# Kernel tuning notes

Hardware: AMD Instinct MI355X
Metric: run time of the kernel (lower is better)

## Reference

```python
import jax, jax.numpy as jnp
import numpy as np
import math

DIM = 1024
HEADS = 16
HEAD_DIM = DIM // HEADS
ROT = min(HEAD_DIM, 32)  # rotary_dim
B, S = 2, 1024


def setup_inputs() -> dict:
    key = jax.random.key(0)
    ks = jax.random.split(key, 32)
    lin = lambda k: jax.random.normal(k, (DIM, DIM), jnp.float32) * 0.02
    bias = lambda k: jax.random.normal(k, (DIM,), jnp.float32) * 0.01
    inp = {
        'real': jax.random.normal(ks[0], (B, S, DIM), jnp.float32),
        'imag': jax.random.normal(ks[1], (B, S, DIM), jnp.float32),
        'Wq_r': lin(ks[2]), 'bq_r': bias(ks[3]),
        'Wk_r': lin(ks[4]), 'bk_r': bias(ks[5]),
        'Wv_r': lin(ks[6]), 'bv_r': bias(ks[7]),
        'Wq_i': lin(ks[8]), 'bq_i': bias(ks[9]),
        'Wk_i': lin(ks[10]), 'bk_i': bias(ks[11]),
        'Wv_i': lin(ks[12]), 'bv_i': bias(ks[13]),
        'Wo_r': lin(ks[14]), 'bo_r': bias(ks[15]),
        'Wo_i': lin(ks[16]), 'bo_i': bias(ks[17]),
        'phase_shifts': jax.random.normal(ks[18], (HEADS, HEAD_DIM), jnp.float32) * 0.02,
        'ent': jnp.eye(HEADS, dtype=jnp.float32) + jax.random.normal(ks[19], (HEADS, HEADS), jnp.float32) * 0.01,
        'rot_freqs': (10000.0 ** (-jnp.arange(0, ROT, 2, dtype=jnp.float32) / ROT)),
        'strength': jnp.ones((1,), jnp.float32),
        'temp': jnp.ones((1,), jnp.float32),
    }
    return inp


def _fwd(real, imag, Wq_r, bq_r, Wk_r, bk_r, Wv_r, bv_r,
         Wq_i, bq_i, Wk_i, bk_i, Wv_i, bv_i,
         Wo_r, bo_r, Wo_i, bo_i,
         phase_shifts, ent, rot_freqs, strength, temp):
    b, s, _ = real.shape
    to_heads = lambda t: t.reshape(b, s, HEADS, HEAD_DIM).transpose(0, 2, 1, 3)  # bhsd
    lin = lambda x, W, bb: x @ W + bb

    q_r = to_heads(lin(real, Wq_r, bq_r))
    k_r = to_heads(lin(real, Wk_r, bk_r))
    v_r = to_heads(lin(real, Wv_r, bv_r))
    q_i = to_heads(lin(imag, Wq_i, bq_i))
    k_i = to_heads(lin(imag, Wk_i, bk_i))
    v_i = to_heads(lin(imag, Wv_i, bv_i))

    # rotary on first ROT dims (pairwise rotation)
    pos = jnp.arange(s, dtype=jnp.float32)
    emb = pos[:, None] * rot_freqs[None, :]           # [S, ROT/2]
    cos = jnp.cos(emb)[None, None]                    # [1,1,S,ROT/2]
    sin = jnp.sin(emb)[None, None]

    def rope(t):
        tr = t[..., :ROT].reshape(b, HEADS, s, ROT // 2, 2)
        r0 = tr[..., 0] * cos - tr[..., 1] * sin
        r1 = tr[..., 1] * cos + tr[..., 0] * sin
        rr = jnp.stack([r0, r1], axis=-1).reshape(b, HEADS, s, ROT)
        return jnp.concatenate([rr, t[..., ROT:]], axis=-1)

    q_r, k_r = rope(q_r), rope(k_r)
    q_i, k_i = rope(q_i), rope(k_i)

    # entanglement mixing across heads
    mix = lambda t: jnp.einsum('bhsd,hx->bxsd', t, ent)
    q_r, q_i, k_r, k_i = mix(q_r), mix(q_i), mix(k_r), mix(k_i)

    # per-head phase shift (complex rotation)
    pc = jnp.cos(phase_shifts)[None, :, None, :]      # [1,H,1,D]
    ps = jnp.sin(phase_shifts)[None, :, None, :]
    q_r, q_i = q_r * pc - q_i * ps, q_r * ps + q_i * pc
    k_r, k_i = k_r * pc - k_i * ps, k_r * ps + k_i * pc

    scale = 1.0 / math.sqrt(HEAD_DIM)
    attn_r = (jnp.einsum('bhqd,bhkd->bhqk', q_r, k_r) + jnp.einsum('bhqd,bhkd->bhqk', q_i, k_i)) * scale
    attn_i = (jnp.einsum('bhqd,bhkd->bhqk', q_i, k_r) - jnp.einsum('bhqd,bhkd->bhqk', q_r, k_i)) * scale
    attn_mag = jnp.sqrt(attn_r ** 2 + attn_i ** 2 + 1e-6)

    causal = jnp.triu(jnp.ones((s, s), dtype=bool), k=1)[None, None]
    attn_mag = jnp.where(causal, -jnp.inf, attn_mag)

    t = jnp.maximum(temp, 0.01)
    g = jax.nn.sigmoid(strength)
    attn = jax.nn.softmax(attn_mag * g / t, axis=-1)

    out_r = jnp.einsum('bhqk,bhkd->bhqd', attn, v_r).transpose(0, 2, 1, 3).reshape(b, s, DIM)
    out_i = jnp.einsum('bhqk,bhkd->bhqd', attn, v_i).transpose(0, 2, 1, 3).reshape(b, s, DIM)
    return lin(out_r, Wo_r, bo_r), lin(out_i, Wo_i, bo_i)


def reference(real, imag, Wq_r, bq_r, Wk_r, bk_r, Wv_r, bv_r,
              Wq_i, bq_i, Wk_i, bk_i, Wv_i, bv_i,
              Wo_r, bo_r, Wo_i, bo_i,
              phase_shifts, ent, rot_freqs, strength, temp):
    return _fwd(real, imag, Wq_r, bq_r, Wk_r, bk_r, Wv_r, bv_r,
                Wq_i, bq_i, Wk_i, bk_i, Wv_i, bv_i,
                Wo_r, bo_r, Wo_i, bo_i,
                phase_shifts, ent, rot_freqs, strength, temp)
```

## Files before the change

### kernel.cpp

```cpp
#include <hip/hip_runtime.h>
#include <stdint.h>

typedef unsigned short u16;
typedef __bf16 bf16x8 __attribute__((ext_vector_type(8)));
typedef float f32x4 __attribute__((ext_vector_type(4)));
typedef unsigned int u32x4 __attribute__((ext_vector_type(4)));

__device__ __forceinline__ u16 f2bf(float f) {
  uint32_t u = __float_as_uint(f);
  u += 0x7FFFu + ((u >> 16) & 1u);
  return (u16)(u >> 16);
}
__device__ __forceinline__ float bf2f(u16 h) {
  return __uint_as_float(((uint32_t)h) << 16);
}
__device__ __forceinline__ float fsqrt(float x) {
  float r; asm("v_sqrt_f32 %0, %1" : "=v"(r) : "v"(x)); return r;
}
__device__ __forceinline__ void gld16(const void* g, void* lds) {
  __builtin_amdgcn_global_load_lds(
      (const __attribute__((address_space(1))) uint32_t*)g,
      (__attribute__((address_space(3))) uint32_t*)lds, 16, 0, 0);
}
__device__ __forceinline__ f32x4 mfma16(u32x4 a, u32x4 b, f32x4 c) {
  return __builtin_amdgcn_mfma_f32_16x16x32_bf16(
      __builtin_bit_cast(bf16x8, a), __builtin_bit_cast(bf16x8, b), c, 0, 0, 0);
}

__global__ __launch_bounds__(256) void tables_kernel(const float* __restrict__ rotf,
                                                     const float* __restrict__ phase,
                                                     float* __restrict__ T) {
  int id = blockIdx.x * 256 + threadIdx.x;
  if (id < 16384) {
    int s = id >> 4, jj = id & 15;
    float sn, cs;
    sincosf((float)s * rotf[jj], &sn, &cs);
    T[id] = cs;
    T[16384 + id] = sn;
  } else if (id < 16384 + 1024) {
    int p = id - 16384;
    float sn, cs;
    sincosf(phase[p], &sn, &cs);
    T[32768 + p] = cs;
    T[33792 + p] = sn;
  }
}

__global__ __launch_bounds__(256) void convx_kernel(const float* __restrict__ real,
                                                    const float* __restrict__ imag,
                                                    u16* __restrict__ Xr,
                                                    u16* __restrict__ Xi) {
  int u = blockIdx.x * 256 + threadIdx.x;
  int a = u >> 18;
  int r = u & 262143;
  int m = r >> 7, slot = r & 127;
  const float* src = (a ? imag : real) + (size_t)m * 1024 + slot * 8;
  int slot2 = (slot & ~7) | ((slot ^ m) & 7);
  u16* dst = (a ? Xi : Xr) + (size_t)m * 1024 + slot2 * 8;
  f32x4 v0 = *(const f32x4*)(src);
  f32x4 v1 = *(const f32x4*)(src + 4);
  union { u16 h[8]; u32x4 v; } o;
#pragma unroll
  for (int e = 0; e < 4; ++e) { o.h[e] = f2bf(v0[e]); o.h[4 + e] = f2bf(v1[e]); }
  *(u32x4*)dst = o.v;
}

__global__ __launch_bounds__(256) void convw_kernel(
    const float* __restrict__ w0, const float* __restrict__ w1,
    const float* __restrict__ w2, const float* __restrict__ w3,
    const float* __restrict__ w4, const float* __restrict__ w5,
    const float* __restrict__ w6, const float* __restrict__ w7,
    u16* __restrict__ WtAll) {
  __shared__ float Lt[64][65];
  int z = blockIdx.z;
  const float* W = (z == 0) ? w0 : (z == 1) ? w1 : (z == 2) ? w2 : (z == 3) ? w3
                 : (z == 4) ? w4 : (z == 5) ? w5 : (z == 6) ? w6 : w7;
  u16* Wt = WtAll + (size_t)z * (1024 * 1024);
  int tid = threadIdx.x;
  int n0 = blockIdx.x * 64, k0 = blockIdx.y * 64;
#pragma unroll
  for (int it = 0; it < 4; ++it) {
    int idx = it * 256 + tid;
    int kr = idx >> 4, nc = (idx & 15) * 4;
    f32x4 v = *(const f32x4*)(W + (size_t)(k0 + kr) * 1024 + n0 + nc);
#pragma unroll
    for (int e = 0; e < 4; ++e) Lt[kr][nc + e] = v[e];
  }
  __syncthreads();
#pragma unroll
  for (int it = 0; it < 2; ++it) {
    int idx = it * 256 + tid;
    int nr = idx >> 3, sl = idx & 7;
    union { u16 h[8]; u32x4 v; } o;
#pragma unroll
    for (int e = 0; e < 8; ++e) o.h[e] = f2bf(Lt[sl * 8 + e][nr]);
    int sl2 = sl ^ (nr & 7);
    *(u32x4*)(Wt + (size_t)(n0 + nr) * 1024 + k0 + sl2 * 8) = o.v;
  }
}

__device__ __forceinline__ void gemm128(const u16* __restrict__ A, const u16* __restrict__ W,
                                        const float* __restrict__ bias,
                                        u16* __restrict__ outB, float* __restrict__ outF) {
  __shared__ __align__(16) u16 As[2][128 * 64];
  __shared__ __align__(16) u16 Bs[2][128 * 64];
  int tid = threadIdx.x, l = tid & 63, w = tid >> 6;
  int lr = l & 15, lh = l >> 4;
  int m0 = blockIdx.y * 128, n0 = blockIdx.x * 128;
  int wr = w >> 1, wc = w & 1;
  f32x4 acc[4][4];
#pragma unroll
  for (int mi = 0; mi < 4; ++mi)
#pragma unroll
    for (int ni = 0; ni < 4; ++ni) acc[mi][ni] = f32x4{0.f, 0.f, 0.f, 0.f};

  const u16* aA = A + (size_t)(m0 + w * 8 + (l >> 3)) * 1024 + (l & 7) * 8;
  const u16* aW = W + (size_t)(n0 + w * 8 + (l >> 3)) * 1024 + (l & 7) * 8;
  int ldoff = w * 1024 + l * 16;

#pragma unroll
  for (int c = 0; c < 4; ++c) {
    gld16(aA + c * 32768, (char*)As[0] + ldoff + c * 4096);
    gld16(aW + c * 32768, (char*)Bs[0] + ldoff + c * 4096);
  }
  __syncthreads();

  for (int kt = 0; kt < 16; ++kt) {
    int cur = kt & 1;
    if (kt < 15) {
      const u16* nA = aA + (kt + 1) * 64;
      const u16* nW = aW + (kt + 1) * 64;
      char* dA = (char*)As[cur ^ 1] + ldoff;
      char* dB = (char*)Bs[cur ^ 1] + ldoff;
#pragma unroll
      for (int c = 0; c < 4; ++c) {
        gld16(nA + c * 32768, dA + c * 4096);
        gld16(nW + c * 32768, dB + c * 4096);
      }
    }
    const char* cA = (const char*)As[cur];
    const char* cB = (const char*)Bs[cur];
#pragma unroll
    for (int kk = 0; kk < 2; ++kk) {
      u32x4 af[4], bf[4];
#pragma unroll
      for (int mi = 0; mi < 4; ++mi) {
        int row = wr * 64 + mi * 16 + lr;
        af[mi] = *(const u32x4*)(cA + row * 128 +
                                 ((kk * 64 + lh * 16) ^ ((row & 7) << 4)));
      }
#pragma unroll
      for (int ni = 0; ni < 4; ++ni) {
        int row = wc * 64 + ni * 16 + lr;
        bf[ni] = *(const u32x4*)(cB + row * 128 +
                                 ((kk * 64 + lh * 16) ^ ((row & 7) << 4)));
      }
#pragma unroll
      for (int mi = 0; mi < 4; ++mi)
#pragma unroll
        for (int ni = 0; ni < 4; ++ni)
          acc[mi][ni] = mfma16(af[mi], bf[ni], acc[mi][ni]);
    }
    __syncthreads();
  }
#pragma unroll
  for (int ni = 0; ni < 4; ++ni) {
    int col = n0 + wc * 64 + ni * 16 + lr;
    float bv = bias[col];
#pragma unroll
    for (int mi = 0; mi < 4; ++mi)
#pragma unroll
      for (int rr = 0; rr < 4; ++rr) {
        int row = m0 + wr * 64 + mi * 16 + 4 * lh + rr;
        float v = acc[mi][ni][rr] + bv;
        if (outF) outF[(size_t)row * 1024 + col] = v;
        else      outB[(size_t)row * 1024 + col] = f2bf(v);
      }
  }
}

__global__ __launch_bounds__(256) void gemm_proj_kernel(
    const u16* __restrict__ Xr, const u16* __restrict__ Xi, const u16* __restrict__ Wt,
    const float* b0, const float* b1, const float* b2,
    const float* b3, const float* b4, const float* b5,
    u16* __restrict__ qkv) {
  int z = blockIdx.z;
  const u16* A = (z < 3) ? Xr : Xi;
  const u16* W = Wt + (size_t)z * (1024 * 1024);
  const float* bias = (z == 0) ? b0 : (z == 1) ? b1 : (z == 2) ? b2
                    : (z == 3) ? b3 : (z == 4) ? b4 : b5;
  u16* out = qkv + (size_t)z * (2048 * 1024);
  gemm128(A, W, bias, out, nullptr);
}

__global__ __launch_bounds__(256) void gemm_out_kernel(
    const u16* __restrict__ O, const u16* __restrict__ Wt2,
    const float* br, const float* bi, float* __restrict__ dout) {
  int z = blockIdx.z;
  gemm128(O + (size_t)z * (2048 * 1024), Wt2 + (size_t)z * (1024 * 1024),
          z ? bi : br, nullptr, dout + (size_t)z * (2048 * 1024));
}

__global__ __launch_bounds__(256) void transform_kernel(
    const u16* __restrict__ qkv, const float* __restrict__ ent,
    const float* __restrict__ T,
    u16* __restrict__ Qr, u16* __restrict__ Qi, u16* __restrict__ Kr,
    u16* __restrict__ Ki, u16* __restrict__ Vr, u16* __restrict__ Vi) {
  __shared__ float Lqr[16][65], Lqi[16][65], Lkr[16][65], Lki[16][65];
  __shared__ float sent[256];
  int tid = threadIdx.x;
  int bs = blockIdx.x;
  int b = bs >> 10, s = bs & 1023;
  sent[tid] = ent[tid];
  const u16* qr_raw = qkv;
  const u16* kr_raw = qkv + (size_t)1 * 2048 * 1024;
  const u16* vr_raw = qkv + (size_t)2 * 2048 * 1024;
  const u16* qi_raw = qkv + (size_t)3 * 2048 * 1024;
  const u16* ki_raw = qkv + (size_t)4 * 2048 * 1024;
  const u16* vi_raw = qkv + (size_t)5 * 2048 * 1024;
  size_t rowoff = (size_t)bs * 1024;
#pragma unroll
  for (int it = 0; it < 2; ++it) {
    int u = it * 256 + tid;
    int hh = u >> 5, j = u & 31;
    int base = hh * 64 + 2 * j;
    uint32_t aqr = *(const uint32_t*)(qr_raw + rowoff + base);
    uint32_t aqi = *(const uint32_t*)(qi_raw + rowoff + base);
    uint32_t akr = *(const uint32_t*)(kr_raw + rowoff + base);
    uint32_t aki = *(const uint32_t*)(ki_raw + rowoff + base);
    float qr0 = bf2f((u16)aqr), qr1 = bf2f((u16)(aqr >> 16));
    float qi0 = bf2f((u16)aqi), qi1 = bf2f((u16)(aqi >> 16));
    float kr0 = bf2f((u16)akr), kr1 = bf2f((u16)(akr >> 16));
    float ki0 = bf2f((u16)aki), ki1 = bf2f((u16)(aki >> 16));
    if (j < 16) {
      float cs = T[s * 16 + j];
      float sn = T[16384 + s * 16 + j];
      float t0;
      t0 = qr0; qr0 = t0 * cs - qr1 * sn; qr1 = qr1 * cs + t0 * sn;
      t0 = qi0; qi0 = t0 * cs - qi1 * sn; qi1 = qi1 * cs + t0 * sn;
      t0 = kr0; kr0 = t0 * cs - kr1 * sn; kr1 = kr1 * cs + t0 * sn;
      t0 = ki0; ki0 = t0 * cs - ki1 * sn; ki1 = ki1 * cs + t0 * sn;
    }
    int d0 = 2 * j;
    Lqr[hh][d0] = qr0; Lqr[hh][d0 + 1] = qr1;
    Lqi[hh][d0] = qi0; Lqi[hh][d0 + 1] = qi1;
    Lkr[hh][d0] = kr0; Lkr[hh][d0 + 1] = kr1;
    Lki[hh][d0] = ki0; Lki[hh][d0 + 1] = ki1;
  }
  __syncthreads();
#pragma unroll
  for (int it = 0; it < 4; ++it) {
    int u = it * 256 + tid;
    int x = u >> 6, d = u & 63;
    float mqr = 0.f, mqi = 0.f, mkr = 0.f, mki = 0.f;
#pragma unroll
    for (int hh = 0; hh < 16; ++hh) {
      float e = sent[hh * 16 + x];
      mqr += Lqr[hh][d] * e; mqi += Lqi[hh][d] * e;
      mkr += Lkr[hh][d] * e; mki += Lki[hh][d] * e;
    }
    float pc_ = T[32768 + x * 64 + d];
    float ps_ = T[33792 + x * 64 + d];
    float oqr = (mqr * pc_ - mqi * ps_) * 0.125f;
    float oqi = (mqr * ps_ + mqi * pc_) * 0.125f;
    float okr = mkr * pc_ - mki * ps_;
    float oki = mkr * ps_ + mki * pc_;
    size_t obase = ((size_t)(b * 16 + x) * 1024 + s) * 64;
    Qr[obase + d] = f2bf(oqr);
    Qi[obase + d] = f2bf(oqi);
    int dsw = (d & 7) | ((((d >> 3) ^ s) & 7) << 3);
    Kr[obase + dsw] = f2bf(okr);
    Ki[obase + dsw] = f2bf(oki);
  }
  {
    int u = tid;
    int comp = u >> 7, hh = (u >> 3) & 15, sl = u & 7;
    const u16* src = comp ? vi_raw : vr_raw;
    u16* dst = comp ? Vi : Vr;
    u32x4 vv = *(const u32x4*)(src + rowoff + hh * 64 + sl * 8);
    *(u32x4*)(dst + ((size_t)(b * 16 + hh) * 1024 + s) * 64 + sl * 8) = vv;
  }
}

__global__ __launch_bounds__(256) void transv_kernel(const u16* __restrict__ Vr,
                                                     const u16* __restrict__ Vi,
                                                     u16* __restrict__ VTr,
                                                     u16* __restrict__ VTi) {
  int bid = blockIdx.x;
  int comp = bid >> 9, bh = (bid >> 4) & 31, t = bid & 15;
  const u16* src = (comp ? Vi : Vr) + ((size_t)bh * 1024 + t * 64) * 64;
  u16* dst = (comp ? VTi : VTr) + (size_t)bh * 65536;
  __shared__ __align__(16) u16 Lt[64][72];
  int tid = threadIdx.x;
#pragma unroll
  for (int it = 0; it < 2; ++it) {
    int i = it * 256 + tid;
    int r = i >> 3, sl = i & 7;
    *(u32x4*)(&Lt[r][sl * 8]) = *(const u32x4*)(src + r * 64 + sl * 8);
  }
  __syncthreads();
#pragma unroll
  for (int it = 0; it < 2; ++it) {
    int i = it * 256 + tid;
    int d = i >> 3, sl = i & 7;
    union { u16 h[8]; u32x4 v; } o;
#pragma unroll
    for (int e = 0; e < 8; ++e) o.h[e] = Lt[sl * 8 + e][d];
    int sl2 = sl ^ (d & 7);
    *(u32x4*)(dst + (size_t)d * 1024 + t * 64 + sl2 * 8) = o.v;
  }
}

__global__ __launch_bounds__(512) void attn_kernel(
    const u16* __restrict__ Qr, const u16* __restrict__ Qi,
    const u16* __restrict__ Kr, const u16* __restrict__ Ki,
    const u16* __restrict__ VTr, const u16* __restrict__ VTi,
    const float* __restrict__ strength, const float* __restrict__ temp,
    u16* __restrict__ por0, u16* __restrict__ por1,
    u16* __restrict__ por2, u16* __restrict__ por3,
    u16* __restrict__ poi0, u16* __restrict__ poi1,
    u16* __restrict__ poi2, u16* __restrict__ poi3,
    float* __restrict__ Pm, float* __restrict__ Pl) {
  __shared__ __align__(16) u16 smem[24576];
  char* sb = (char*)smem;
  const int PO = 32768;
  int tid = threadIdx.x, l = tid & 63, w = tid >> 6;
  int lr = l & 15, lh = l >> 4;
  int id = blockIdx.x;
  int x = id & 7, j = id >> 3;
  int bh = x + 8 * (j & 3);
  int cc = j >> 2;
  int qbi, sp;
  if (cc < 8)       { qbi = 7 - (cc >> 2); sp = cc & 3; }
  else if (cc < 14) { int r = cc - 8; int q3 = r / 3; qbi = 5 - q3; sp = r - 3 * q3; }
  else if (cc < 18) { int r = cc - 14; qbi = 3 - (r >> 1); sp = r & 1; }
  else              { qbi = 19 - cc; sp = 0; }
  int q0 = qbi * 128;
  int nt = 2 * qbi + 2;
  int t0 = sp * 4, t1 = min(nt, t0 + 4);
  int b = bh >> 4; (void)b;
  u16* POr = (sp == 0) ? por0 : (sp == 1) ? por1 : (sp == 2) ? por2 : por3;
  u16* POi = (sp == 0) ? poi0 : (sp == 1) ? poi1 : (sp == 2) ? poi2 : poi3;

  float g = 1.f / (1.f + __expf(-strength[0]));
  float tt = fmaxf(temp[0], 0.01f);
  float gt = g / tt;

  size_t qbase = ((size_t)bh * 1024 + q0 + w * 16 + lr) * 64 + lh * 8;
  u32x4 qrF[2], qiF[2], nqrF[2];
#pragma unroll
  for (int kk = 0; kk < 2; ++kk) {
    qrF[kk] = *(const u32x4*)(Qr + qbase + kk * 32);
    qiF[kk] = *(const u32x4*)(Qi + qbase + kk * 32);
    nqrF[kk] = qrF[kk] ^ 0x80008000u;
  }
  f32x4 o_r[4], o_i[4];
#pragma unroll
  for (int n = 0; n < 4; ++n) { o_r[n] = f32x4{0,0,0,0}; o_i[n] = f32x4{0,0,0,0}; }
  float m_run[4], l_run[4];
#pragma unroll
  for (int rr = 0; rr < 4; ++rr) { m_run[rr] = -__builtin_inff(); l_run[rr] = 0.f; }

  int role = w >> 1;
  int pl = ((w & 1) << 6) | l;
  const u16* gsrc;
  if (role < 2) {
    gsrc = (role ? Ki : Kr) + ((size_t)bh * 1024 + t0 * 64) * 64 + pl * 8;
  } else {
    gsrc = (role == 3 ? VTi : VTr) + (size_t)bh * 65536 + t0 * 64 +
           (pl >> 3) * 1024 + (pl & 7) * 8;
  }
  char* ldst = sb + role * 8192 + pl * 16;

  for (int t = t0; t < t1; ++t) {
    if (role < 2) {
#pragma unroll
      for (int c = 0; c < 4; ++c) gld16(gsrc + c * 1024, ldst + c * 2048);
      gsrc += 4096;
    } else {
#pragma unroll
      for (int c = 0; c < 4; ++c) gld16(gsrc + c * 16384, ldst + c * 2048);
      gsrc += 64;
    }
    __syncthreads();

    f32x4 sr[4], si[4];
#pragma unroll
    for (int n = 0; n < 4; ++n) { sr[n] = f32x4{0,0,0,0}; si[n] = f32x4{0,0,0,0}; }
#pragma unroll
    for (int kk = 0; kk < 2; ++kk) {
#pragma unroll
      for (int n = 0; n < 4; ++n) {
        int kv = n * 16 + lr;
        int xoff = (kk * 64 + lh * 16) ^ ((kv & 7) << 4);
        u32x4 fkr = *(const u32x4*)(sb + kv * 128 + xoff);
        u32x4 fki = *(const u32x4*)(sb + 8192 + kv * 128 + xoff);
        sr[n] = mfma16(qrF[kk], fkr, sr[n]);
        sr[n] = mfma16(qiF[kk], fki, sr[n]);
        si[n] = mfma16(qiF[kk], fkr, si[n]);
        si[n] = mfma16(nqrF[kk], fki, si[n]);
      }
    }

    float pl_[4][4], pm[4];
#pragma unroll
    for (int rr = 0; rr < 4; ++rr) pm[rr] = -__builtin_inff();
    bool diag = (t >= 2 * qbi);
#pragma unroll
    for (int n = 0; n < 4; ++n)
#pragma unroll
      for (int rr = 0; rr < 4; ++rr) {
        float a = sr[n][rr], ci = si[n][rr];
        float mag = fsqrt(a * a + ci * ci + 1e-6f) * gt;
        if (diag) {
          int colg = t * 64 + n * 16 + lr;
          int rowg = q0 + w * 16 + 4 * lh + rr;
          if (colg > rowg) mag = -__builtin_inff();
        }
        pl_[n][rr] = mag;
        pm[rr] = fmaxf(pm[rr], mag);
      }
#pragma unroll
    for (int mk = 1; mk <= 8; mk <<= 1)
#pragma unroll
      for (int rr = 0; rr < 4; ++rr)
        pm[rr] = fmaxf(pm[rr], __shfl_xor(pm[rr], mk));

    bool defer = true;
#pragma unroll
    for (int rr = 0; rr < 4; ++rr) defer = defer && (pm[rr] - m_run[rr] <= 8.f);
    bool noresc = __all(defer ? 1 : 0);
    float fr[4];
    if (!noresc) {
#pragma unroll
      for (int rr = 0; rr < 4; ++rr) {
        float mnew = fmaxf(m_run[rr], pm[rr]);
        fr[rr] = __expf(m_run[rr] - mnew);
        m_run[rr] = mnew;
      }
    }
    float rs[4];
#pragma unroll
    for (int rr = 0; rr < 4; ++rr) rs[rr] = 0.f;
#pragma unroll
    for (int n = 0; n < 4; ++n)
#pragma unroll
      for (int rr = 0; rr < 4; ++rr) {
        float p = __expf(pl_[n][rr] - m_run[rr]);
        pl_[n][rr] = p;
        rs[rr] += p;
      }
#pragma unroll
    for (int mk = 1; mk <= 8; mk <<= 1)
#pragma unroll
      for (int rr = 0; rr < 4; ++rr)
        rs[rr] += __shfl_xor(rs[rr], mk);
    if (!noresc) {
#pragma unroll
      for (int rr = 0; rr < 4; ++rr) l_run[rr] = l_run[rr] * fr[rr] + rs[rr];
#pragma unroll
      for (int n = 0; n < 4; ++n)
#pragma unroll
        for (int rr = 0; rr < 4; ++rr) { o_r[n][rr] *= fr[rr]; o_i[n][rr] *= fr[rr]; }
    } else {
#pragma unroll
      for (int rr = 0; rr < 4; ++rr) l_run[rr] += rs[rr];
    }

    char* pw = sb + PO + w * 2048;
#pragma unroll
    for (int n = 0; n < 4; ++n)
#pragma unroll
      for (int rr = 0; rr < 4; ++rr) {
        int row = 4 * lh + rr, col = n * 16 + lr;
        int by = row * 128 + ((col & 7) * 2) + ((((col >> 3) ^ row) & 7) << 4);
        *(u16*)(pw + by) = f2bf(pl_[n][rr]);
      }
    u32x4 pf[2];
#pragma unroll
    for (int kk = 0; kk < 2; ++kk)
      pf[kk] = *(const u32x4*)(pw + lr * 128 + ((kk * 64 + lh * 16) ^ ((lr & 7) << 4)));
#pragma unroll
    for (int kk = 0; kk < 2; ++kk)
#pragma unroll
      for (int n = 0; n < 4; ++n) {
        int dl = n * 16 + lr;
        int xoff = (kk * 64 + lh * 16) ^ ((dl & 7) << 4);
        u32x4 fvr = *(const u32x4*)(sb + 16384 + dl * 128 + xoff);
        u32x4 fvi = *(const u32x4*)(sb + 24576 + dl * 128 + xoff);
        o_r[n] = mfma16(pf[kk], fvr, o_r[n]);
        o_i[n] = mfma16(pf[kk], fvi, o_i[n]);
      }
    __syncthreads();
  }

  size_t pbase = ((size_t)bh * 1024 + q0 + w * 16 + 4 * lh) * 64;
#pragma unroll
  for (int n = 0; n < 4; ++n)
#pragma unroll
    for (int rr = 0; rr < 4; ++rr) {
      POr[pbase + rr * 64 + n * 16 + lr] = f2bf(o_r[n][rr]);
      POi[pbase + rr * 64 + n * 16 + lr] = f2bf(o_i[n][rr]);
    }
  if (lr == 0) {
    size_t mbase = (size_t)sp * 32768 + (size_t)bh * 1024 + q0 + w * 16 + 4 * lh;
#pragma unroll
    for (int rr = 0; rr < 4; ++rr) {
      Pm[mbase + rr] = m_run[rr];
      Pl[mbase + rr] = l_run[rr];
    }
  }
}

__global__ __launch_bounds__(256) void combine_kernel(
    const u16* __restrict__ por0, const u16* __restrict__ por1,
    const u16* __restrict__ por2, const u16* __restrict__ por3,
    const u16* __restrict__ poi0, const u16* __restrict__ poi1,
    const u16* __restrict__ poi2, const u16* __restrict__ poi3,
    const float* __restrict__ Pm, const float* __restrict__ Pl,
    u16* __restrict__ Or, u16* __restrict__ Oi) {
  int bid = blockIdx.x;
  int bh = bid >> 4, rg = bid & 15;
  int b = bh >> 4, h = bh & 15;
  int ns = (rg >> 2) + 1;
  int tid = threadIdx.x;
  int row = tid >> 2, q = tid & 3;
  int s = rg * 64 + row;
  size_t ro = (size_t)bh * 1024 + s;
  const u16* PR[4] = {por0, por1, por2, por3};
  const u16* PI[4] = {poi0, poi1, poi2, poi3};
  float msp[4], lsp[4], csw[4];
  float M = -__builtin_inff();
#pragma unroll
  for (int sp = 0; sp < 4; ++sp) {
    if (sp < ns) {
      msp[sp] = Pm[ro + (size_t)sp * 32768];
      lsp[sp] = Pl[ro + (size_t)sp * 32768];
      M = fmaxf(M, msp[sp]);
    }
  }
  float lt = 0.f;
#pragma unroll
  for (int sp = 0; sp < 4; ++sp) {
    if (sp < ns) { csw[sp] = __expf(msp[sp] - M); lt += lsp[sp] * csw[sp]; }
    else csw[sp] = 0.f;
  }
  float inv = 1.f / lt;
#pragma unroll
  for (int sp = 0; sp < 4; ++sp) csw[sp] *= inv;
  size_t obase = ro * 64;
#pragma unroll
  for (int g = 0; g < 2; ++g) {
    int d = q * 16 + g * 8;
    float accr[8], acci[8];
#pragma unroll
    for (int e = 0; e < 8; ++e) { accr[e] = 0.f; acci[e] = 0.f; }
#pragma unroll
    for (int sp = 0; sp < 4; ++sp) {
      if (sp < ns) {
        union { u16 h[8]; u32x4 v; } ar, ai;
        ar.v = *(const u32x4*)(PR[sp] + obase + d);
        ai.v = *(const u32x4*)(PI[sp] + obase + d);
#pragma unroll
        for (int e = 0; e < 8; ++e) {
          accr[e] += csw[sp] * bf2f(ar.h[e]);
          acci[e] += csw[sp] * bf2f(ai.h[e]);
        }
      }
    }
    union { u16 h[8]; u32x4 v; } outr, outi;
#pragma unroll
    for (int e = 0; e < 8; ++e) { outr.h[e] = f2bf(accr[e]); outi.h[e] = f2bf(acci[e]); }
    int slot2 = (d >> 3) ^ (s & 7);
    size_t oo = ((size_t)b * 1024 + s) * 1024 + h * 64 + slot2 * 8;
    *(u32x4*)(Or + oo) = outr.v;
    *(u32x4*)(Oi + oo) = outi.v;
  }
}

extern "C" void kernel_launch(void* const* d_in, const int* in_sizes, int n_in,
                              void* d_out, int out_size, void* d_ws, size_t ws_size,
                              hipStream_t stream) {
  (void)in_sizes; (void)n_in; (void)out_size; (void)ws_size;
  const float* real = (const float*)d_in[0];
  const float* imag = (const float*)d_in[1];
  const float* bq_r = (const float*)d_in[3];
  const float* bk_r = (const float*)d_in[5];
  const float* bv_r = (const float*)d_in[7];
  const float* bq_i = (const float*)d_in[9];
  const float* bk_i = (const float*)d_in[11];
  const float* bv_i = (const float*)d_in[13];
  const float* bo_r = (const float*)d_in[15];
  const float* bo_i = (const float*)d_in[17];
  const float* phase = (const float*)d_in[18];
  const float* ent = (const float*)d_in[19];
  const float* rotf = (const float*)d_in[20];
  const float* strength = (const float*)d_in[21];
  const float* temp = (const float*)d_in[22];

  u16* ws = (u16*)d_ws;
  const size_t M1 = 1024 * 1024, M2 = 2048 * 1024;
  u16* Xr  = ws;
  u16* Xi  = Xr + M2;
  u16* Wt  = Xi + M2;
  u16* qkv = Wt + 8 * M1;
  u16* Qr  = qkv + 6 * M2;
  u16* Qi  = Qr + M2;
  u16* Kr  = Qi + M2;
  u16* Ki  = Kr + M2;
  u16* Vr  = Ki + M2;
  u16* Vi  = Vr + M2;
  u16* VTr = Vi + M2;
  u16* VTi = VTr + M2;
  u16* Or  = VTi + M2;
  u16* Oi  = Or + M2;
  u16* por0 = qkv;
  u16* por1 = qkv + M2;
  u16* por2 = qkv + 2 * M2;
  u16* por3 = qkv + 3 * M2;
  u16* poi0 = qkv + 4 * M2;
  u16* poi1 = qkv + 5 * M2;
  u16* poi2 = Vr;
  u16* poi3 = Vi;
  float* Pm = (float*)Xr;
  float* Pl = Pm + 131072;
  float* TBL = (float*)Oi;

  tables_kernel<<<68, 256, 0, stream>>>(rotf, phase, TBL);
  convx_kernel<<<2048, 256, 0, stream>>>(real, imag, Xr, Xi);
  convw_kernel<<<dim3(16, 16, 8), 256, 0, stream>>>(
      (const float*)d_in[2],  (const float*)d_in[4],  (const float*)d_in[6],
      (const float*)d_in[8],  (const float*)d_in[10], (const float*)d_in[12],
      (const float*)d_in[14], (const float*)d_in[16], Wt);
  gemm_proj_kernel<<<dim3(8, 16, 6), 256, 0, stream>>>(Xr, Xi, Wt, bq_r, bk_r, bv_r,
                                                       bq_i, bk_i, bv_i, qkv);
  transform_kernel<<<2048, 256, 0, stream>>>(qkv, ent, TBL, Qr, Qi, Kr, Ki, Vr, Vi);
  transv_kernel<<<1024, 256, 0, stream>>>(Vr, Vi, VTr, VTi);
  attn_kernel<<<640, 512, 0, stream>>>(Qr, Qi, Kr, Ki, VTr, VTi, strength, temp,
                                       por0, por1, por2, por3,
                                       poi0, poi1, poi2, poi3, Pm, Pl);
  combine_kernel<<<512, 256, 0, stream>>>(por0, por1, por2, por3,
                                          poi0, poi1, poi2, poi3, Pm, Pl, Or, Oi);
  gemm_out_kernel<<<dim3(8, 16, 2), 256, 0, stream>>>(Or, Wt + 6 * M1, bo_r, bo_i,
                                                      (float*)d_out);
}
```

Baseline: 164.9 us.

## Double-buffer attention K/V tiles, use exp2 softmax, single-buffer GEMM tiles

The attention kernel now double-buffers its K/V tiles in LDS, prefetching the next tile before computing on the current one. It uses manual vmcnt waits and raw s_barrier in place of __syncthreads. Softmax moves to base-2 via v_exp_f32 with a log2e-prescaled logit, and P is converted to bf16 with the hardware pack instruction. The GEMM drops its LDS double buffer and loads each k-tile synchronously, which saves LDS but exposes global-load latency. The deferred-rescale threshold is rescaled to base 2, and the extra LDS in attention may lower occupancy.

```diff
diff --git a/kernel.cpp b/kernel.cpp
--- a/kernel.cpp
+++ b/kernel.cpp
@@ -16,6 +16,14 @@
 }
 __device__ __forceinline__ float fsqrt(float x) {
   float r; asm("v_sqrt_f32 %0, %1" : "=v"(r) : "v"(x)); return r;
+}
+__device__ __forceinline__ float fexp2(float x) {
+  float r; asm("v_exp_f32 %0, %1" : "=v"(r) : "v"(x)); return r;
+}
+__device__ __forceinline__ u16 cvt_bf16(float x) {
+  uint32_t r;
+  asm("v_cvt_pk_bf16_f32 %0, %1, %2" : "=v"(r) : "v"(x), "v"(x));
+  return (u16)r;
 }
 __device__ __forceinline__ void gld16(const void* g, void* lds) {
   __builtin_amdgcn_global_load_lds(
@@ -102,8 +110,8 @@
 __device__ __forceinline__ void gemm128(const u16* __restrict__ A, const u16* __restrict__ W,
                                         const float* __restrict__ bias,
                                         u16* __restrict__ outB, float* __restrict__ outF) {
-  __shared__ __align__(16) u16 As[2][128 * 64];
-  __shared__ __align__(16) u16 Bs[2][128 * 64];
+  __shared__ __align__(16) u16 As[128 * 64];
+  __shared__ __align__(16) u16 Bs[128 * 64];
   int tid = threadIdx.x, l = tid & 63, w = tid >> 6;
   int lr = l & 15, lh = l >> 4;
   int m0 = blockIdx.y * 128, n0 = blockIdx.x * 128;
@@ -114,45 +122,29 @@
 #pragma unroll
     for (int ni = 0; ni < 4; ++ni) acc[mi][ni] = f32x4{0.f, 0.f, 0.f, 0.f};
 
-  const u16* aA = A + (size_t)(m0 + w * 8 + (l >> 3)) * 1024 + (l & 7) * 8;
-  const u16* aW = W + (size_t)(n0 + w * 8 + (l >> 3)) * 1024 + (l & 7) * 8;
-  int ldoff = w * 1024 + l * 16;
-
-#pragma unroll
-  for (int c = 0; c < 4; ++c) {
-    gld16(aA + c * 32768, (char*)As[0] + ldoff + c * 4096);
-    gld16(aW + c * 32768, (char*)Bs[0] + ldoff + c * 4096);
-  }
-  __syncthreads();
-
   for (int kt = 0; kt < 16; ++kt) {
-    int cur = kt & 1;
-    if (kt < 15) {
-      const u16* nA = aA + (kt + 1) * 64;
-      const u16* nW = aW + (kt + 1) * 64;
-      char* dA = (char*)As[cur ^ 1] + ldoff;
-      char* dB = (char*)Bs[cur ^ 1] + ldoff;
-#pragma unroll
-      for (int c = 0; c < 4; ++c) {
-        gld16(nA + c * 32768, dA + c * 4096);
-        gld16(nW + c * 32768, dB + c * 4096);
-      }
-    }
-    const char* cA = (const char*)As[cur];
-    const char* cB = (const char*)Bs[cur];
+#pragma unroll
+    for (int c = 0; c < 4; ++c) {
+      int chunk = c * 4 + w;
+      int i = chunk * 64 + l;
+      int row = i >> 3, off = i & 7;
+      gld16(A + (size_t)(m0 + row) * 1024 + kt * 64 + off * 8, (char*)As + chunk * 1024);
+      gld16(W + (size_t)(n0 + row) * 1024 + kt * 64 + off * 8, (char*)Bs + chunk * 1024);
+    }
+    __syncthreads();
 #pragma unroll
     for (int kk = 0; kk < 2; ++kk) {
       u32x4 af[4], bf[4];
 #pragma unroll
       for (int mi = 0; mi < 4; ++mi) {
         int row = wr * 64 + mi * 16 + lr;
-        af[mi] = *(const u32x4*)(cA + row * 128 +
+        af[mi] = *(const u32x4*)((const char*)As + row * 128 +
                                  ((kk * 64 + lh * 16) ^ ((row & 7) << 4)));
       }
 #pragma unroll
       for (int ni = 0; ni < 4; ++ni) {
         int row = wc * 64 + ni * 16 + lr;
-        bf[ni] = *(const u32x4*)(cB + row * 128 +
+        bf[ni] = *(const u32x4*)((const char*)Bs + row * 128 +
                                  ((kk * 64 + lh * 16) ^ ((row & 7) << 4)));
       }
 #pragma unroll
@@ -321,9 +313,9 @@
     u16* __restrict__ poi0, u16* __restrict__ poi1,
     u16* __restrict__ poi2, u16* __restrict__ poi3,
     float* __restrict__ Pm, float* __restrict__ Pl) {
-  __shared__ __align__(16) u16 smem[24576];
+  __shared__ __align__(16) u16 smem[40960];
   char* sb = (char*)smem;
-  const int PO = 32768;
+  const int PO = 65536;
   int tid = threadIdx.x, l = tid & 63, w = tid >> 6;
   int lr = l & 15, lh = l >> 4;
   int id = blockIdx.x;
@@ -338,13 +330,12 @@
   int q0 = qbi * 128;
   int nt = 2 * qbi + 2;
   int t0 = sp * 4, t1 = min(nt, t0 + 4);
-  int b = bh >> 4; (void)b;
   u16* POr = (sp == 0) ? por0 : (sp == 1) ? por1 : (sp == 2) ? por2 : por3;
   u16* POi = (sp == 0) ? poi0 : (sp == 1) ? poi1 : (sp == 2) ? poi2 : poi3;
 
   float g = 1.f / (1.f + __expf(-strength[0]));
   float tt = fmaxf(temp[0], 0.01f);
-  float gt = g / tt;
+  float gt2 = g / tt * 1.4426950408889634f;
 
   size_t qbase = ((size_t)bh * 1024 + q0 + w * 16 + lr) * 64 + lh * 8;
   u32x4 qrF[2], qiF[2], nqrF[2];
@@ -370,19 +361,32 @@
     gsrc = (role == 3 ? VTi : VTr) + (size_t)bh * 65536 + t0 * 64 +
            (pl >> 3) * 1024 + (pl & 7) * 8;
   }
-  char* ldst = sb + role * 8192 + pl * 16;
-
-  for (int t = t0; t < t1; ++t) {
+  char* ldbase = sb + role * 8192 + pl * 16;
+
+  auto stage = [&](int bufsel) {
+    char* dst = ldbase + bufsel * 32768;
     if (role < 2) {
 #pragma unroll
-      for (int c = 0; c < 4; ++c) gld16(gsrc + c * 1024, ldst + c * 2048);
+      for (int c = 0; c < 4; ++c) gld16(gsrc + c * 1024, dst + c * 2048);
       gsrc += 4096;
     } else {
 #pragma unroll
-      for (int c = 0; c < 4; ++c) gld16(gsrc + c * 16384, ldst + c * 2048);
+      for (int c = 0; c < 4; ++c) gld16(gsrc + c * 16384, dst + c * 2048);
       gsrc += 64;
     }
-    __syncthreads();
+  };
+
+  stage(0);
+
+  for (int t = t0; t < t1; ++t) {
+    int cur = (t - t0) & 1;
+    bool pf = (t + 1 < t1);
+    if (pf) stage(cur ^ 1);
+    if (pf) asm volatile("s_waitcnt vmcnt(4)" ::: "memory");
+    else    asm volatile("s_waitcnt vmcnt(0)" ::: "memory");
+    __builtin_amdgcn_sched_barrier(0);
+    asm volatile("s_barrier" ::: "memory");
+    char* kb = sb + cur * 32768;
 
     f32x4 sr[4], si[4];
 #pragma unroll
@@ -393,8 +397,8 @@
       for (int n = 0; n < 4; ++n) {
         int kv = n * 16 + lr;
         int xoff = (kk * 64 + lh * 16) ^ ((kv & 7) << 4);
-        u32x4 fkr = *(const u32x4*)(sb + kv * 128 + xoff);
-        u32x4 fki = *(const u32x4*)(sb + 8192 + kv * 128 + xoff);
+        u32x4 fkr = *(const u32x4*)(kb + kv * 128 + xoff);
+        u32x4 fki = *(const u32x4*)(kb + 8192 + kv * 128 + xoff);
         sr[n] = mfma16(qrF[kk], fkr, sr[n]);
         sr[n] = mfma16(qiF[kk], fki, sr[n]);
         si[n] = mfma16(qiF[kk], fkr, si[n]);
@@ -411,7 +415,7 @@
 #pragma unroll
       for (int rr = 0; rr < 4; ++rr) {
         float a = sr[n][rr], ci = si[n][rr];
-        float mag = fsqrt(a * a + ci * ci + 1e-6f) * gt;
+        float mag = fsqrt(a * a + ci * ci + 1e-6f) * gt2;
         if (diag) {
           int colg = t * 64 + n * 16 + lr;
           int rowg = q0 + w * 16 + 4 * lh + rr;
@@ -428,14 +432,14 @@
 
     bool defer = true;
 #pragma unroll
-    for (int rr = 0; rr < 4; ++rr) defer = defer && (pm[rr] - m_run[rr] <= 8.f);
+    for (int rr = 0; rr < 4; ++rr) defer = defer && (pm[rr] - m_run[rr] <= 11.54f);
     bool noresc = __all(defer ? 1 : 0);
     float fr[4];
     if (!noresc) {
 #pragma unroll
       for (int rr = 0; rr < 4; ++rr) {
         float mnew = fmaxf(m_run[rr], pm[rr]);
-        fr[rr] = __expf(m_run[rr] - mnew);
+        fr[rr] = fexp2(m_run[rr] - mnew);
         m_run[rr] = mnew;
       }
     }
@@ -446,7 +450,7 @@
     for (int n = 0; n < 4; ++n)
 #pragma unroll
       for (int rr = 0; rr < 4; ++rr) {
-        float p = __expf(pl_[n][rr] - m_run[rr]);
+        float p = fexp2(pl_[n][rr] - m_run[rr]);
         pl_[n][rr] = p;
         rs[rr] += p;
       }
@@ -474,24 +478,24 @@
       for (int rr = 0; rr < 4; ++rr) {
         int row = 4 * lh + rr, col = n * 16 + lr;
         int by = row * 128 + ((col & 7) * 2) + ((((col >> 3) ^ row) & 7) << 4);
-        *(u16*)(pw + by) = f2bf(pl_[n][rr]);
-      }
-    u32x4 pf[2];
+        *(u16*)(pw + by) = cvt_bf16(pl_[n][rr]);
+      }
+    u32x4 pf2[2];
 #pragma unroll
     for (int kk = 0; kk < 2; ++kk)
-      pf[kk] = *(const u32x4*)(pw + lr * 128 + ((kk * 64 + lh * 16) ^ ((lr & 7) << 4)));
+      pf2[kk] = *(const u32x4*)(pw + lr * 128 + ((kk * 64 + lh * 16) ^ ((lr & 7) << 4)));
 #pragma unroll
     for (int kk = 0; kk < 2; ++kk)
 #pragma unroll
       for (int n = 0; n < 4; ++n) {
         int dl = n * 16 + lr;
         int xoff = (kk * 64 + lh * 16) ^ ((dl & 7) << 4);
-        u32x4 fvr = *(const u32x4*)(sb + 16384 + dl * 128 + xoff);
-        u32x4 fvi = *(const u32x4*)(sb + 24576 + dl * 128 + xoff);
-        o_r[n] = mfma16(pf[kk], fvr, o_r[n]);
-        o_i[n] = mfma16(pf[kk], fvi, o_i[n]);
-      }
-    __syncthreads();
+        u32x4 fvr = *(const u32x4*)(kb + 16384 + dl * 128 + xoff);
+        u32x4 fvi = *(const u32x4*)(kb + 24576 + dl * 128 + xoff);
+        o_r[n] = mfma16(pf2[kk], fvr, o_r[n]);
+        o_i[n] = mfma16(pf2[kk], fvi, o_i[n]);
+      }
+    asm volatile("s_barrier" ::: "memory");
   }
 
   size_t pbase = ((size_t)bh * 1024 + q0 + w * 16 + 4 * lh) * 64;
@@ -542,7 +546,7 @@
   float lt = 0.f;
 #pragma unroll
   for (int sp = 0; sp < 4; ++sp) {
-    if (sp < ns) { csw[sp] = __expf(msp[sp] - M); lt += lsp[sp] * csw[sp]; }
+    if (sp < ns) { csw[sp] = fexp2(msp[sp] - M); lt += lsp[sp] * csw[sp]; }
     else csw[sp] = 0.f;
   }
   float inv = 1.f / lt;
```

New measurement: 162.2 us. No clear change (-1.6%).
